# Performance work log

Hardware: AMD Instinct MI355X
Metric: run time of the kernel (lower is better)

The kernel has to match this reference:

```python
import jax, jax.numpy as jnp
import numpy as np

N = 50000      # nodes
E = 800000     # edges
IN = 16        # embedding_dimension
HID = 128      # hidden_dimension
OUT = 3        # out_dim
R = 2          # relation_num
NEG_SLOPE = 0.2  # PyG RGATConv default negative_slope


def setup_inputs() -> dict:
    key = jax.random.key(0)
    ks = jax.random.split(key, 9)
    feature = jax.random.normal(ks[0], (N, IN), jnp.float32)
    edge_index = jax.random.randint(ks[1], (2, E), 0, N, jnp.int32)
    edge_type = jax.random.randint(ks[2], (E,), 0, R, jnp.int32)
    # RGATConv params (heads=1): weight [R, in, out], q/k [out, 1], bias [out]
    W1 = jax.random.normal(ks[3], (R, IN, HID), jnp.float32) * (1.0 / np.sqrt(IN))
    q1 = jax.random.normal(ks[4], (HID, 1), jnp.float32) * (1.0 / np.sqrt(HID))
    k1 = jax.random.normal(ks[5], (HID, 1), jnp.float32) * (1.0 / np.sqrt(HID))
    b1 = jnp.zeros((HID,), jnp.float32)
    W2 = jax.random.normal(ks[6], (R, HID, OUT), jnp.float32) * (1.0 / np.sqrt(HID))
    q2 = jax.random.normal(ks[7], (OUT, 1), jnp.float32) * (1.0 / np.sqrt(OUT))
    k2 = jax.random.normal(ks[8], (OUT, 1), jnp.float32) * (1.0 / np.sqrt(OUT))
    b2 = jnp.zeros((OUT,), jnp.float32)
    return dict(feature=feature, edge_index=edge_index, edge_type=edge_type,
                W1=W1, q1=q1, k1=k1, b1=b1, W2=W2, q2=q2, k2=k2, b2=b2)


def rgat_conv(x, src, dst, edge_type, W, q, k, b, n_nodes):
    # Per-relation node transform once at node level: [R, N, C]
    # (equivalent to per-edge bmm with W[edge_type] in PyG, but avoids
    #  gathering [E, in, C] weight matrices)
    xr = jnp.einsum('nd,rdc->rnc', x, W)
    out_i = xr[edge_type, dst]  # target node transformed by edge relation, [E, C]
    out_j = xr[edge_type, src]  # source node transformed by edge relation, [E, C]
    # additive self-attention, heads=1: alpha = leaky_relu(q(x_i) + k(x_j))
    alpha = jax.nn.leaky_relu((out_i @ q + out_j @ k)[:, 0], NEG_SLOPE)  # [E]
    # across-relation softmax over incoming edges of each target node
    m = jax.ops.segment_max(alpha, dst, num_segments=n_nodes)
    ex = jnp.exp(alpha - m[dst])
    denom = jax.ops.segment_sum(ex, dst, num_segments=n_nodes)
    a = ex / (denom[dst] + 1e-16)
    # message = alpha * W_r x_j, scatter-sum to target nodes
    out = jax.ops.segment_sum(out_j * a[:, None], dst, num_segments=n_nodes)
    return out + b


def reference(feature, edge_index, edge_type, W1, q1, k1, b1, W2, q2, k2, b2):
    src, dst = edge_index[0], edge_index[1]  # PyG: row 0 = source j, row 1 = target i
    h = rgat_conv(feature, src, dst, edge_type, W1, q1, k1, b1, N)
    # F.dropout(p=0.3) is identity in eval mode
    out = rgat_conv(h, src, dst, edge_type, W2, q2, k2, b2, N)
    return out
```

## Files before the change

### kernel.cpp

```cpp
#include <hip/hip_runtime.h>
#include <math.h>

#define IN_DIM 16
#define HID 128
#define NEG 0.2f

__device__ __forceinline__ float lrelu(float a) { return a > 0.f ? a : NEG * a; }

__global__ void __launch_bounds__(256) k_pre(
    const float* __restrict__ W1, const float* __restrict__ q1, const float* __restrict__ k1,
    const float* __restrict__ b1, const float* __restrict__ W2, const float* __restrict__ q2,
    const float* __restrict__ k2,
    float* __restrict__ wq1, float* __restrict__ wk1,
    float* __restrict__ M, float* __restrict__ C,
    int* __restrict__ counts, int n_nodes) {
    int zi = blockIdx.x * 256 + threadIdx.x;
    if (zi < n_nodes) counts[zi] = 0;

    int w = blockIdx.x * 4 + (threadIdx.x >> 6);
    if (w >= 362) return;
    int lane = threadIdx.x & 63;

    auto T = [&](int c, int o) -> float {
        if (o < 3) return W2[c * 3 + o];
        if (o < 6) return W2[384 + c * 3 + (o - 3)];
        const float* base = (o == 6 || o == 8) ? (W2 + c * 3) : (W2 + 384 + c * 3);
        const float* v = (o < 8) ? q2 : k2;
        return base[0] * v[0] + base[1] * v[1] + base[2] * v[2];
    };

    if (w < 330) {
        bool isC = (w >= 320);
        int o  = isC ? (w - 320) : (w % 10);
        int dp = isC ? 0 : (w / 10);
        float acc = 0.f;
        for (int c = lane; c < HID; c += 64) {
            float left = isC ? b1[c] : W1[dp * HID + c];
            acc += left * T(c, o);
        }
#pragma unroll
        for (int off = 32; off; off >>= 1) acc += __shfl_xor(acc, off);
        if (lane == 0) { if (isC) C[o] = acc; else M[dp * 10 + o] = acc; }
    } else {
        int i = w - 330;
        float aq = 0.f, ak = 0.f;
        for (int c = lane; c < HID; c += 64) {
            float wv = W1[i * HID + c];
            aq += wv * q1[c]; ak += wv * k1[c];
        }
#pragma unroll
        for (int off = 32; off; off >>= 1) { aq += __shfl_xor(aq, off); ak += __shfl_xor(ak, off); }
        if (lane == 0) { wq1[i] = aq; wk1[i] = ak; }
    }
}

__global__ void __launch_bounds__(256) k_prep(
    const float* __restrict__ x,
    const float* __restrict__ wq1, const float* __restrict__ wk1,
    float* __restrict__ sq1, float* __restrict__ sk1,
    const int* __restrict__ dstp, int* __restrict__ counts, int* __restrict__ rank,
    int n_nodes, int ecnt) {
    __shared__ float wq[2 * IN_DIM], wk[2 * IN_DIM];
    if (threadIdx.x < 2 * IN_DIM) { wq[threadIdx.x] = wq1[threadIdx.x]; wk[threadIdx.x] = wk1[threadIdx.x]; }
    __syncthreads();
    int gid = blockIdx.x * 256 + threadIdx.x;
    if (gid < ecnt) rank[gid] = atomicAdd(&counts[dstp[gid]], 1);
    if (gid < n_nodes) {
        float q0 = 0.f, q1v = 0.f, k0 = 0.f, k1v = 0.f;
        const float4* xp = reinterpret_cast<const float4*>(x + (size_t)gid * IN_DIM);
#pragma unroll
        for (int d4 = 0; d4 < IN_DIM / 4; ++d4) {
            float4 v = xp[d4];
            float vv[4] = {v.x, v.y, v.z, v.w};
#pragma unroll
            for (int j = 0; j < 4; ++j) {
                int d = d4 * 4 + j;
                q0 += vv[j] * wq[d]; q1v += vv[j] * wq[IN_DIM + d];
                k0 += vv[j] * wk[d]; k1v += vv[j] * wk[IN_DIM + d];
            }
        }
        sq1[gid] = q0; sq1[n_nodes + gid] = q1v;
        sk1[gid] = k0; sk1[n_nodes + gid] = k1v;
    }
}

__global__ void k_scan1(const int* __restrict__ counts, int* __restrict__ exoff,
                        int* __restrict__ blockSums, int n) {
    __shared__ int s[512];
    int tid = threadIdx.x;
    int gid = blockIdx.x * 512 + tid;
    int v = (gid < n) ? counts[gid] : 0;
    s[tid] = v;
    __syncthreads();
    for (int off = 1; off < 512; off <<= 1) {
        int t = (tid >= off) ? s[tid - off] : 0;
        __syncthreads();
        s[tid] += t;
        __syncthreads();
    }
    if (gid < n) exoff[gid] = s[tid] - v;
    if (tid == 511) blockSums[blockIdx.x] = s[511];
}

__global__ void k_scan2(const int* __restrict__ blockSums, int* __restrict__ blockBase, int nblk) {
    __shared__ int s[128];
    int t = threadIdx.x;
    int v = (t < nblk) ? blockSums[t] : 0;
    s[t] = v;
    __syncthreads();
    for (int off = 1; off < 128; off <<= 1) {
        int u = (t >= off) ? s[t - off] : 0;
        __syncthreads();
        s[t] += u;
        __syncthreads();
    }
    if (t < nblk) blockBase[t] = s[t] - v;
}

__global__ void k_scan3(const int* __restrict__ exoff, const int* __restrict__ blockBase,
                        int* __restrict__ offsets, int n_nodes, int ecnt) {
    int i = blockIdx.x * 256 + threadIdx.x;
    if (i < n_nodes) offsets[i] = exoff[i] + blockBase[i >> 9];
    if (i == 0) offsets[n_nodes] = ecnt;
}

__global__ void __launch_bounds__(256) k_scatter(
    const int* __restrict__ srcp, const int* __restrict__ dstp,
    const int* __restrict__ etp, const int* __restrict__ offsets,
    const int* __restrict__ rank, int* __restrict__ sorted, int ecnt) {
    int e = blockIdx.x * 256 + threadIdx.x;
    if (e >= ecnt) return;
    int d = dstp[e];
    sorted[offsets[d] + rank[e]] = (etp[e] << 16) | srcp[e];
}

__global__ void __launch_bounds__(256) k_layer1(
    const int* __restrict__ offsets, const int* __restrict__ sorted,
    const float* __restrict__ sq1, const float* __restrict__ sk1,
    const float* __restrict__ x, const float* __restrict__ M, const float* __restrict__ C,
    float* __restrict__ xr2p, float* __restrict__ sq2, float* __restrict__ sk2,
    int n_nodes) {
    __shared__ float Ml[320], Cl[10];
    __shared__ float Al[4][32];
    for (int i = threadIdx.x; i < 320; i += 256) Ml[i] = M[i];
    if (threadIdx.x < 10)  Cl[threadIdx.x] = C[threadIdx.x];
    __syncthreads();
    int wid = threadIdx.x >> 6, lane = threadIdx.x & 63;
    int n = blockIdx.x * 4 + wid;
    if (n >= n_nodes) return;
    int beg = offsets[n], end = offsets[n + 1];
    float s0 = sq1[n], s1 = sq1[n_nodes + n];
    int d = lane & 15, j = lane >> 4;
    float a0 = 0.f, a1 = 0.f, ds = 0.f;
    for (int e = beg + j; e < end; e += 4) {
        int pk = sorted[e];
        int et = pk >> 16, s = pk & 0xFFFF;
        float w = __expf(lrelu((et ? s1 : s0) + sk1[et * n_nodes + s]));
        ds += w;
        float xv = x[s * IN_DIM + d];
        if (et == 0) a0 += w * xv; else a1 += w * xv;
    }
#pragma unroll
    for (int off = 16; off <= 32; off <<= 1) {
        a0 += __shfl_xor(a0, off);
        a1 += __shfl_xor(a1, off);
        ds += __shfl_xor(ds, off);
    }
    float inv = 1.f / (ds + 1e-16f);
    if (lane < 16) { Al[wid][lane] = a0 * inv; Al[wid][16 + lane] = a1 * inv; }
    if (lane < 10) {
        float acc = Cl[lane];
#pragma unroll
        for (int dp = 0; dp < 32; ++dp) acc += Al[wid][dp] * Ml[dp * 10 + lane];
        int o = lane;
        if (o < 3)       xr2p[(size_t)n * 4 + o] = acc;
        else if (o < 6)  xr2p[((size_t)n_nodes + n) * 4 + (o - 3)] = acc;
        else if (o == 6) sq2[n] = acc;
        else if (o == 7) sq2[n_nodes + n] = acc;
        else if (o == 8) sk2[n] = acc;
        else             sk2[n_nodes + n] = acc;
    }
}

__global__ void __launch_bounds__(256) k_node2(
    const int* __restrict__ offsets, const int* __restrict__ sorted,
    const float* __restrict__ sq2, const float* __restrict__ sk2,
    const float* __restrict__ xr2p, const float* __restrict__ b2,
    float* __restrict__ out, int n_nodes) {
    int gid = blockIdx.x * 256 + threadIdx.x;
    int n = gid >> 4;
    int l = threadIdx.x & 15;
    if (n >= n_nodes) return;
    int beg = offsets[n], end = offsets[n + 1];
    if (beg == end) {
        if (l < 3) out[(size_t)n * 3 + l] = b2[l];
        return;
    }
    float s0 = sq2[n], s1 = sq2[n_nodes + n];
    float lsum = 0.f, a0 = 0.f, a1 = 0.f, a2 = 0.f;
    for (int e = beg + l; e < end; e += 16) {
        int pk = sorted[e];
        int et = pk >> 16, s = pk & 0xFFFF;
        float w = __expf(lrelu((et ? s1 : s0) + sk2[et * n_nodes + s]));
        lsum += w;
        const float4 xr = *reinterpret_cast<const float4*>(xr2p + ((size_t)et * n_nodes + s) * 4);
        a0 += w * xr.x; a1 += w * xr.y; a2 += w * xr.z;
    }
#pragma unroll
    for (int off = 8; off; off >>= 1) {
        lsum += __shfl_xor(lsum, off);
        a0 += __shfl_xor(a0, off);
        a1 += __shfl_xor(a1, off);
        a2 += __shfl_xor(a2, off);
    }
    if (l == 0) {
        float inv = 1.f / (lsum + 1e-16f);
        out[(size_t)n * 3 + 0] = a0 * inv + b2[0];
        out[(size_t)n * 3 + 1] = a1 * inv + b2[1];
        out[(size_t)n * 3 + 2] = a2 * inv + b2[2];
    }
}

extern "C" void kernel_launch(void* const* d_in, const int* in_sizes, int n_in,
                              void* d_out, int out_size, void* d_ws, size_t ws_size,
                              hipStream_t stream) {
    const float* x  = (const float*)d_in[0];
    const int*   ei = (const int*)d_in[1];
    const int*   etp = (const int*)d_in[2];
    const float* W1 = (const float*)d_in[3];
    const float* q1 = (const float*)d_in[4];
    const float* k1 = (const float*)d_in[5];
    const float* b1 = (const float*)d_in[6];
    const float* W2 = (const float*)d_in[7];
    const float* q2 = (const float*)d_in[8];
    const float* k2 = (const float*)d_in[9];
    const float* b2 = (const float*)d_in[10];
    float* out = (float*)d_out;

    const int n_nodes = in_sizes[0] / IN_DIM;
    const int ecnt    = in_sizes[2];
    const int* srcp = ei;
    const int* dstp = ei + ecnt;

    char* wp = (char*)d_ws;
    auto alloc = [&](size_t bytes) -> char* {
        char* p = wp;
        wp += (bytes + 255) & ~(size_t)255;
        return p;
    };
    float* xr2p  = (float*)alloc((size_t)2 * n_nodes * 4 * 4);
    float* sq1   = (float*)alloc((size_t)2 * n_nodes * 4);
    float* sk1   = (float*)alloc((size_t)2 * n_nodes * 4);
    float* sq2   = (float*)alloc((size_t)2 * n_nodes * 4);
    float* sk2   = (float*)alloc((size_t)2 * n_nodes * 4);
    float* wq1   = (float*)alloc(32 * 4);
    float* wk1   = (float*)alloc(32 * 4);
    float* Mbuf  = (float*)alloc(320 * 4);
    float* Cbuf  = (float*)alloc(10 * 4);
    int* counts  = (int*)alloc((size_t)n_nodes * 4);
    int* exoff   = (int*)alloc((size_t)n_nodes * 4);
    int* blockSums = (int*)alloc(512);
    int* blockBase = (int*)alloc(512);
    int* offsets = (int*)alloc((size_t)(n_nodes + 1) * 4);
    int* rank    = (int*)alloc((size_t)ecnt * 4);
    int* sorted  = (int*)alloc((size_t)ecnt * 4);

    int nblk = (n_nodes + 255) / 256;
    int eblk = (ecnt + 255) / 256;
    int nblk_scan = (n_nodes + 511) / 512;

    k_pre<<<nblk, 256, 0, stream>>>(W1, q1, k1, b1, W2, q2, k2, wq1, wk1, Mbuf, Cbuf,
                                    counts, n_nodes);
    k_prep<<<eblk, 256, 0, stream>>>(x, wq1, wk1, sq1, sk1, dstp, counts, rank, n_nodes, ecnt);
    k_scan1<<<nblk_scan, 512, 0, stream>>>(counts, exoff, blockSums, n_nodes);
    k_scan2<<<1, 128, 0, stream>>>(blockSums, blockBase, nblk_scan);
    k_scan3<<<(n_nodes + 256) / 256, 256, 0, stream>>>(exoff, blockBase, offsets, n_nodes, ecnt);
    k_scatter<<<eblk, 256, 0, stream>>>(srcp, dstp, etp, offsets, rank, sorted, ecnt);

    k_layer1<<<(n_nodes + 3) / 4, 256, 0, stream>>>(offsets, sorted, sq1, sk1, x, Mbuf, Cbuf,
                                                    xr2p, sq2, sk2, n_nodes);
    k_node2<<<(n_nodes * 16 + 255) / 256, 256, 0, stream>>>(offsets, sorted, sq2, sk2, xr2p, b2, out, n_nodes);
}
```

Measured before the change: 111.5 us.

## Fuse scan passes via last-block ticket and pack layer-2 key score into xr2p

Merges the three-kernel prefix scan into one kernel: the last block to finish, found with an atomic ticket, scans the block sums. Every consumer now computes offsets on the fly from exoff plus blockBase instead of reading a materialised offsets array. The layer-2 key scores go into the unused fourth lane of the xr2p float4, so one gather returns both features and score, and sq2 is interleaved so it loads as a float2. This removes two kernel launches and a separate random gather per edge, at the cost of an extra indirection when reading offsets and a threadfence/atomic handshake.

Result: slower. 122.2 us (+9.6%).

```diff
diff --git a/kernel.cpp b/kernel.cpp
--- a/kernel.cpp
+++ b/kernel.cpp
@@ -6,6 +6,12 @@
 #define NEG 0.2f
 
 __device__ __forceinline__ float lrelu(float a) { return a > 0.f ? a : NEG * a; }
+
+__device__ __forceinline__ int off_at(const int* __restrict__ exoff,
+                                      const int* __restrict__ blockBase,
+                                      int i, int n_nodes, int ecnt) {
+    return (i >= n_nodes) ? ecnt : (exoff[i] + blockBase[i >> 9]);
+}
 
 __global__ void __launch_bounds__(256) k_pre(
     const float* __restrict__ W1, const float* __restrict__ q1, const float* __restrict__ k1,
@@ -13,9 +19,10 @@
     const float* __restrict__ k2,
     float* __restrict__ wq1, float* __restrict__ wk1,
     float* __restrict__ M, float* __restrict__ C,
-    int* __restrict__ counts, int n_nodes) {
+    int* __restrict__ counts, int* __restrict__ ticket, int n_nodes) {
     int zi = blockIdx.x * 256 + threadIdx.x;
     if (zi < n_nodes) counts[zi] = 0;
+    if (zi == 0) *ticket = 0;
 
     int w = blockIdx.x * 4 + (threadIdx.x >> 6);
     if (w >= 362) return;
@@ -84,9 +91,12 @@
     }
 }
 
-__global__ void k_scan1(const int* __restrict__ counts, int* __restrict__ exoff,
-                        int* __restrict__ blockSums, int n) {
+__global__ void __launch_bounds__(512) k_scan1(
+    const int* __restrict__ counts, int* __restrict__ exoff,
+    int* __restrict__ blockSums, int* __restrict__ blockBase,
+    int* __restrict__ ticket, int n, int nblk) {
     __shared__ int s[512];
+    __shared__ int isLast;
     int tid = threadIdx.x;
     int gid = blockIdx.x * 512 + tid;
     int v = (gid < n) ? counts[gid] : 0;
@@ -100,46 +110,42 @@
     }
     if (gid < n) exoff[gid] = s[tid] - v;
     if (tid == 511) blockSums[blockIdx.x] = s[511];
-}
-
-__global__ void k_scan2(const int* __restrict__ blockSums, int* __restrict__ blockBase, int nblk) {
-    __shared__ int s[128];
-    int t = threadIdx.x;
-    int v = (t < nblk) ? blockSums[t] : 0;
-    s[t] = v;
+    __threadfence();
+    if (tid == 0) isLast = (atomicAdd(ticket, 1) == (int)gridDim.x - 1);
+    __syncthreads();
+    if (!isLast) return;
+    __threadfence();
+    int bv = (tid < nblk) ? blockSums[tid] : 0;
+    s[tid] = bv;
     __syncthreads();
     for (int off = 1; off < 128; off <<= 1) {
-        int u = (t >= off) ? s[t - off] : 0;
-        __syncthreads();
-        s[t] += u;
-        __syncthreads();
-    }
-    if (t < nblk) blockBase[t] = s[t] - v;
-}
-
-__global__ void k_scan3(const int* __restrict__ exoff, const int* __restrict__ blockBase,
-                        int* __restrict__ offsets, int n_nodes, int ecnt) {
-    int i = blockIdx.x * 256 + threadIdx.x;
-    if (i < n_nodes) offsets[i] = exoff[i] + blockBase[i >> 9];
-    if (i == 0) offsets[n_nodes] = ecnt;
+        int u = (tid >= off) ? s[tid - off] : 0;
+        __syncthreads();
+        s[tid] += u;
+        __syncthreads();
+    }
+    if (tid < nblk) blockBase[tid] = s[tid] - bv;
 }
 
 __global__ void __launch_bounds__(256) k_scatter(
     const int* __restrict__ srcp, const int* __restrict__ dstp,
-    const int* __restrict__ etp, const int* __restrict__ offsets,
+    const int* __restrict__ etp,
+    const int* __restrict__ exoff, const int* __restrict__ blockBase,
     const int* __restrict__ rank, int* __restrict__ sorted, int ecnt) {
     int e = blockIdx.x * 256 + threadIdx.x;
     if (e >= ecnt) return;
     int d = dstp[e];
-    sorted[offsets[d] + rank[e]] = (etp[e] << 16) | srcp[e];
+    int o = exoff[d] + blockBase[d >> 9];
+    sorted[o + rank[e]] = (etp[e] << 16) | srcp[e];
 }
 
 __global__ void __launch_bounds__(256) k_layer1(
-    const int* __restrict__ offsets, const int* __restrict__ sorted,
+    const int* __restrict__ exoff, const int* __restrict__ blockBase,
+    const int* __restrict__ sorted,
     const float* __restrict__ sq1, const float* __restrict__ sk1,
     const float* __restrict__ x, const float* __restrict__ M, const float* __restrict__ C,
-    float* __restrict__ xr2p, float* __restrict__ sq2, float* __restrict__ sk2,
-    int n_nodes) {
+    float* __restrict__ xr2p, float* __restrict__ sq2,
+    int n_nodes, int ecnt) {
     __shared__ float Ml[320], Cl[10];
     __shared__ float Al[4][32];
     for (int i = threadIdx.x; i < 320; i += 256) Ml[i] = M[i];
@@ -148,7 +154,8 @@
     int wid = threadIdx.x >> 6, lane = threadIdx.x & 63;
     int n = blockIdx.x * 4 + wid;
     if (n >= n_nodes) return;
-    int beg = offsets[n], end = offsets[n + 1];
+    int beg = off_at(exoff, blockBase, n, n_nodes, ecnt);
+    int end = off_at(exoff, blockBase, n + 1, n_nodes, ecnt);
     float s0 = sq1[n], s1 = sq1[n_nodes + n];
     int d = lane & 15, j = lane >> 4;
     float a0 = 0.f, a1 = 0.f, ds = 0.f;
@@ -175,35 +182,37 @@
         int o = lane;
         if (o < 3)       xr2p[(size_t)n * 4 + o] = acc;
         else if (o < 6)  xr2p[((size_t)n_nodes + n) * 4 + (o - 3)] = acc;
-        else if (o == 6) sq2[n] = acc;
-        else if (o == 7) sq2[n_nodes + n] = acc;
-        else if (o == 8) sk2[n] = acc;
-        else             sk2[n_nodes + n] = acc;
+        else if (o == 6) sq2[2 * n] = acc;
+        else if (o == 7) sq2[2 * n + 1] = acc;
+        else if (o == 8) xr2p[(size_t)n * 4 + 3] = acc;
+        else             xr2p[((size_t)n_nodes + n) * 4 + 3] = acc;
     }
 }
 
 __global__ void __launch_bounds__(256) k_node2(
-    const int* __restrict__ offsets, const int* __restrict__ sorted,
-    const float* __restrict__ sq2, const float* __restrict__ sk2,
-    const float* __restrict__ xr2p, const float* __restrict__ b2,
-    float* __restrict__ out, int n_nodes) {
+    const int* __restrict__ exoff, const int* __restrict__ blockBase,
+    const int* __restrict__ sorted,
+    const float* __restrict__ sq2, const float* __restrict__ xr2p,
+    const float* __restrict__ b2, float* __restrict__ out,
+    int n_nodes, int ecnt) {
     int gid = blockIdx.x * 256 + threadIdx.x;
     int n = gid >> 4;
     int l = threadIdx.x & 15;
     if (n >= n_nodes) return;
-    int beg = offsets[n], end = offsets[n + 1];
+    int beg = off_at(exoff, blockBase, n, n_nodes, ecnt);
+    int end = off_at(exoff, blockBase, n + 1, n_nodes, ecnt);
     if (beg == end) {
         if (l < 3) out[(size_t)n * 3 + l] = b2[l];
         return;
     }
-    float s0 = sq2[n], s1 = sq2[n_nodes + n];
+    const float2 sq = *reinterpret_cast<const float2*>(sq2 + 2 * n);
     float lsum = 0.f, a0 = 0.f, a1 = 0.f, a2 = 0.f;
     for (int e = beg + l; e < end; e += 16) {
         int pk = sorted[e];
         int et = pk >> 16, s = pk & 0xFFFF;
-        float w = __expf(lrelu((et ? s1 : s0) + sk2[et * n_nodes + s]));
+        const float4 xr = *reinterpret_cast<const float4*>(xr2p + ((size_t)et * n_nodes + s) * 4);
+        float w = __expf(lrelu((et ? sq.y : sq.x) + xr.w));
         lsum += w;
-        const float4 xr = *reinterpret_cast<const float4*>(xr2p + ((size_t)et * n_nodes + s) * 4);
         a0 += w * xr.x; a1 += w * xr.y; a2 += w * xr.z;
     }
 #pragma unroll
@@ -252,7 +261,6 @@
     float* sq1   = (float*)alloc((size_t)2 * n_nodes * 4);
     float* sk1   = (float*)alloc((size_t)2 * n_nodes * 4);
     float* sq2   = (float*)alloc((size_t)2 * n_nodes * 4);
-    float* sk2   = (float*)alloc((size_t)2 * n_nodes * 4);
     float* wq1   = (float*)alloc(32 * 4);
     float* wk1   = (float*)alloc(32 * 4);
     float* Mbuf  = (float*)alloc(320 * 4);
@@ -261,7 +269,7 @@
     int* exoff   = (int*)alloc((size_t)n_nodes * 4);
     int* blockSums = (int*)alloc(512);
     int* blockBase = (int*)alloc(512);
-    int* offsets = (int*)alloc((size_t)(n_nodes + 1) * 4);
+    int* ticket  = (int*)alloc(256);
     int* rank    = (int*)alloc((size_t)ecnt * 4);
     int* sorted  = (int*)alloc((size_t)ecnt * 4);
 
@@ -270,14 +278,14 @@
     int nblk_scan = (n_nodes + 511) / 512;
 
     k_pre<<<nblk, 256, 0, stream>>>(W1, q1, k1, b1, W2, q2, k2, wq1, wk1, Mbuf, Cbuf,
-                                    counts, n_nodes);
+                                    counts, ticket, n_nodes);
     k_prep<<<eblk, 256, 0, stream>>>(x, wq1, wk1, sq1, sk1, dstp, counts, rank, n_nodes, ecnt);
-    k_scan1<<<nblk_scan, 512, 0, stream>>>(counts, exoff, blockSums, n_nodes);
-    k_scan2<<<1, 128, 0, stream>>>(blockSums, blockBase, nblk_scan);
-    k_scan3<<<(n_nodes + 256) / 256, 256, 0, stream>>>(exoff, blockBase, offsets, n_nodes, ecnt);
-    k_scatter<<<eblk, 256, 0, stream>>>(srcp, dstp, etp, offsets, rank, sorted, ecnt);
-
-    k_layer1<<<(n_nodes + 3) / 4, 256, 0, stream>>>(offsets, sorted, sq1, sk1, x, Mbuf, Cbuf,
-                                                    xr2p, sq2, sk2, n_nodes);
-    k_node2<<<(n_nodes * 16 + 255) / 256, 256, 0, stream>>>(offsets, sorted, sq2, sk2, xr2p, b2, out, n_nodes);
-}
+    k_scan1<<<nblk_scan, 512, 0, stream>>>(counts, exoff, blockSums, blockBase, ticket,
+                                           n_nodes, nblk_scan);
+    k_scatter<<<eblk, 256, 0, stream>>>(srcp, dstp, etp, exoff, blockBase, rank, sorted, ecnt);
+
+    k_layer1<<<(n_nodes + 3) / 4, 256, 0, stream>>>(exoff, blockBase, sorted, sq1, sk1, x,
+                                                    Mbuf, Cbuf, xr2p, sq2, n_nodes, ecnt);
+    k_node2<<<(n_nodes * 16 + 255) / 256, 256, 0, stream>>>(exoff, blockBase, sorted, sq2,
+                                                            xr2p, b2, out, n_nodes, ecnt);
+}
```
